# Kernel tuning notes

Hardware: AMD Instinct MI355X
Metric: run time of the kernel (lower is better)

## Reference

```python
import jax, jax.numpy as jnp
import numpy as np

EMB = 128
N_RBF = 16
N_EDGES = 1_000_000
N_ATOMS = 50_000


def setup_inputs() -> dict:
    key = jax.random.key(0)
    ks = jax.random.split(key, 16)
    inp = {
        "x": jax.random.normal(ks[0], (N_EDGES, EMB), dtype=jnp.float32),
        "rbf": jax.random.normal(ks[1], (N_EDGES, N_RBF), dtype=jnp.float32),
        "idnb_i": jax.random.randint(ks[2], (N_EDGES,), 0, N_ATOMS, dtype=jnp.int32),
        "n_atoms": N_ATOMS,
        # learned params
        "W_x": jax.random.normal(ks[3], (EMB, EMB), dtype=jnp.float32) * 0.05,
        "b_x": jnp.zeros((EMB,), dtype=jnp.float32),
        "W_rbf": jax.random.normal(ks[4], (N_RBF, EMB), dtype=jnp.float32) * 0.2,
        "b_rbf": jnp.zeros((EMB,), dtype=jnp.float32),
        "W1": jax.random.normal(ks[5], (EMB, EMB), dtype=jnp.float32) * 0.05,
        "b1": jnp.zeros((EMB,), dtype=jnp.float32),
        "W2": jax.random.normal(ks[6], (EMB, EMB), dtype=jnp.float32) * 0.05,
        "b2": jnp.zeros((EMB,), dtype=jnp.float32),
        "W3": jax.random.normal(ks[7], (EMB, EMB), dtype=jnp.float32) * 0.05,
        "b3": jnp.zeros((EMB,), dtype=jnp.float32),
        "W_final": jax.random.normal(ks[8], (EMB, 1), dtype=jnp.float32) * 0.05,
        # scale coefficients (shape [1] as in the keras layer)
        "coef_rbf_a": jnp.exp(jax.random.normal(ks[9], (1,)) * 0.01),
        "coef_rbf_b": jnp.exp(jax.random.normal(ks[10], (1,)) * 0.01),
        "coef_x": jnp.exp(jax.random.normal(ks[11], (1,)) * 0.01),
        "coef_final": jnp.exp(jax.random.normal(ks[12], (1,)) * 0.01),
    }
    return inp


def reference(x, rbf, idnb_i, n_atoms, W_x, b_x, W_rbf, b_rbf, W1, b1, W2, b2,
              W3, b3, W_final, coef_rbf_a, coef_rbf_b, coef_x, coef_final):
    act = jax.nn.silu  # keras 'swish'
    rbf = coef_rbf_a * rbf
    h = act(x @ W_x + b_x)                      # [E, emb]
    g = act(rbf @ W_rbf + b_rbf)                # [E, emb]
    conv_x = (coef_rbf_b * g) * (coef_x * h)    # fused elementwise gate
    a = jax.ops.segment_sum(conv_x, idnb_i, num_segments=n_atoms)  # [n_atoms, emb]
    a = act(a @ W1 + b1)
    a = act(a @ W2 + b2)
    a = act(a @ W3 + b3)
    out = (a @ W_final) * coef_final            # [n_atoms, 1]
    return out
```

## Files before the change

kernel.cpp:

```cpp
#include <hip/hip_runtime.h>

#define E_TOTAL 1000000
#define EMB     128
#define NRBF    16
#define NATOMS  50000
#define APB     16
#define NBLK    ((NATOMS + 255) / 256)

typedef _Float16 f16x8 __attribute__((ext_vector_type(8)));
typedef _Float16 f16x4 __attribute__((ext_vector_type(4)));
typedef float    f32x4 __attribute__((ext_vector_type(4)));

__device__ __forceinline__ float silu_f(float v) {
    return v * (1.0f / (1.0f + __expf(-v)));
}

__device__ __forceinline__ int sigma64(int e) {
    return (((e & 15) >> 2) << 4) + ((e >> 4) << 2) + (e & 3);
}

__global__ __launch_bounds__(256)
void hist_kernel(const int* __restrict__ idnb, int* __restrict__ counts) {
    const int e = blockIdx.x * 256 + threadIdx.x;
    if (e < E_TOTAL) atomicAdd(&counts[idnb[e]], 1);
}

__global__ __launch_bounds__(256)
void scan1_kernel(const int* __restrict__ counts, int* __restrict__ row_ptr,
                  int* __restrict__ bsums) {
    __shared__ int sd[256];
    const int tid = threadIdx.x;
    const int idx = blockIdx.x * 256 + tid;
    const int v = (idx < NATOMS) ? counts[idx] : 0;
    sd[tid] = v;
    __syncthreads();
#pragma unroll
    for (int off = 1; off < 256; off <<= 1) {
        const int t = (tid >= off) ? sd[tid - off] : 0;
        __syncthreads();
        sd[tid] += t;
        __syncthreads();
    }
    if (idx < NATOMS) row_ptr[idx] = sd[tid] - v;
    if (tid == 255) bsums[blockIdx.x] = sd[255];
}

__global__ __launch_bounds__(256)
void scan2_kernel(int* __restrict__ bsums) {
    __shared__ int sd[256];
    const int tid = threadIdx.x;
    const int v = (tid < NBLK) ? bsums[tid] : 0;
    sd[tid] = v;
    __syncthreads();
#pragma unroll
    for (int off = 1; off < 256; off <<= 1) {
        const int t = (tid >= off) ? sd[tid - off] : 0;
        __syncthreads();
        sd[tid] += t;
        __syncthreads();
    }
    if (tid < NBLK) bsums[tid] = sd[tid] - v;
}

__global__ __launch_bounds__(256)
void scan3_kernel(const int* __restrict__ bsums, int* __restrict__ row_ptr,
                  int* __restrict__ cursor) {
    const int idx = blockIdx.x * 256 + threadIdx.x;
    if (idx < NATOMS) {
        const int r = row_ptr[idx] + bsums[blockIdx.x];
        row_ptr[idx] = r;
        cursor[idx]  = r;
    }
    if (idx == 0) row_ptr[NATOMS] = E_TOTAL;
}

__global__ __launch_bounds__(256)
void scatter_kernel(const int* __restrict__ idnb, int* __restrict__ cursor,
                    int* __restrict__ eidx, int* __restrict__ aidxs) {
    const int e = blockIdx.x * 256 + threadIdx.x;
    if (e < E_TOTAL) {
        const int a = idnb[e];
        const int p = atomicAdd(&cursor[a], 1);
        eidx[p]  = e;
        aidxs[p] = a;
    }
}

__global__ __launch_bounds__(256, 2)
void edge_kernel(const float* __restrict__ x,
                 const float* __restrict__ rbf,
                 const int*   __restrict__ eidx,
                 const int*   __restrict__ aidxs,
                 const int*   __restrict__ row_ptr,
                 const float* __restrict__ Wx,
                 const float* __restrict__ bx,
                 const float* __restrict__ Wr,
                 const float* __restrict__ br,
                 const float* __restrict__ c_a,
                 const float* __restrict__ c_b,
                 const float* __restrict__ c_x,
                 float* __restrict__ acc)
{
    __shared__ _Float16 sX[2][64 * 128];
    __shared__ _Float16 sR[2][64 * 40];
    __shared__ float    sAcc[APB][132];
    __shared__ int      sAid[2][64];

    const int tid  = threadIdx.x;
    const int w    = tid >> 6;
    const int lane = tid & 63;
    const int lq   = lane >> 4;
    const int lm   = lane & 15;

    const int aBase = blockIdx.x * APB;
    const int eBeg  = row_ptr[aBase];
    const int eEnd  = row_ptr[aBase + APB];
    const int nEdge = eEnd - eBeg;
    const int ntile = (nEdge + 63) >> 6;

    const float ca = c_a[0];
    const float sc = c_b[0] * c_x[0];
    const int col0 = w * 32 + lm;
    const int col1 = col0 + 16;
    const float bx0 = bx[col0], bx1 = bx[col1];
    const float br0 = br[col0], br1 = br[col1];

    f16x8 wxh[4][2], wxl[4][2], wrh[2], wrl[2];
#pragma unroll
    for (int ks = 0; ks < 4; ++ks)
#pragma unroll
        for (int nt = 0; nt < 2; ++nt) {
            const int n = w * 32 + nt * 16 + lm;
            f16x8 h8, l8;
#pragma unroll
            for (int j = 0; j < 8; ++j) {
                const int k = ks * 32 + lq * 8 + j;
                const float v = Wx[k * EMB + n];
                const _Float16 hv = (_Float16)v;
                h8[j] = hv;
                l8[j] = (_Float16)(v - (float)hv);
            }
            wxh[ks][nt] = h8;
            wxl[ks][nt] = l8;
        }
#pragma unroll
    for (int nt = 0; nt < 2; ++nt) {
        const int n = w * 32 + nt * 16 + lm;
        f16x8 h8, l8;
#pragma unroll
        for (int j = 0; j < 8; ++j) {
            const int k = lq * 8 + j;
            const float v = (k < NRBF) ? Wr[k * EMB + n] : 0.f;
            const _Float16 hv = (_Float16)v;
            h8[j] = hv;
            l8[j] = (_Float16)(v - (float)hv);
        }
        wrh[nt] = h8;
        wrl[nt] = l8;
    }

    for (int f = tid; f < APB * 132; f += 256) ((float*)sAcc)[f] = 0.f;
    for (int f = tid; f < 64 * 24; f += 256) {
        sR[0][(f / 24) * 40 + 16 + (f % 24)] = (_Float16)0.f;
        sR[1][(f / 24) * 40 + 16 + (f % 24)] = (_Float16)0.f;
    }

    float4 px[8];
    float4 pr;
    int    prel = -1;

    auto prefetch = [&](int t) {
        const int nb = eBeg + t * 64;
#pragma unroll
        for (int i = 0; i < 8; ++i) {
            const int e = (tid >> 5) + i * 8;
            const int eid = eidx[min(nb + sigma64(e), eEnd - 1)];
            px[i] = *(const float4*)(x + (size_t)eid * EMB + (tid & 31) * 4);
        }
        {
            const int er = tid >> 2;
            const int eid = eidx[min(nb + sigma64(er), eEnd - 1)];
            pr = *(const float4*)(rbf + (size_t)eid * NRBF + (tid & 3) * 4);
        }
        if (tid < 64) prel = (nb + tid < eEnd) ? (aidxs[nb + tid] - aBase) : -1;
    };

    auto write_lds = [&](int buf) {
#pragma unroll
        for (int i = 0; i < 8; ++i) {
            const int e = (tid >> 5) + i * 8;
            const int kb = (tid & 31) * 4;
            const int idx = (e * 128 + kb) ^ ((e & 7) << 3);
            f16x4 h4 = {(_Float16)px[i].x, (_Float16)px[i].y,
                        (_Float16)px[i].z, (_Float16)px[i].w};
            *(f16x4*)&sX[buf][idx] = h4;
        }
        {
            const int er = tid >> 2;
            const int kb = (tid & 3) * 4;
            f16x4 r4 = {(_Float16)(pr.x * ca), (_Float16)(pr.y * ca),
                        (_Float16)(pr.z * ca), (_Float16)(pr.w * ca)};
            *(f16x4*)&sR[buf][er * 40 + kb] = r4;
        }
        if (tid < 64) sAid[buf][tid] = prel;
    };

    if (ntile > 0) {
        prefetch(0);
        write_lds(0);
        if (ntile > 1) prefetch(1);
    }
    __syncthreads();

    for (int t = 0; t < ntile; ++t) {
        const int cur = t & 1;
        const _Float16* sXc = sX[cur];
        const _Float16* sRc = sR[cur];
        const int*      sAc = sAid[cur];

        int   curA = -2;
        float a0v = 0.f, a1v = 0.f;

#pragma unroll
        for (int mt = 0; mt < 4; ++mt) {
            f32x4 hac[2], gac[2];
#pragma unroll
            for (int nt = 0; nt < 2; ++nt) { hac[nt] = 0.f; gac[nt] = 0.f; }

            const int m = mt * 16 + lm;
            const f16x8 rh = *(const f16x8*)&sRc[m * 40 + lq * 8];
#pragma unroll
            for (int nt = 0; nt < 2; ++nt) {
                gac[nt] = __builtin_amdgcn_mfma_f32_16x16x32_f16(rh, wrh[nt], gac[nt], 0, 0, 0);
                gac[nt] = __builtin_amdgcn_mfma_f32_16x16x32_f16(rh, wrl[nt], gac[nt], 0, 0, 0);
            }
#pragma unroll
            for (int ks = 0; ks < 4; ++ks) {
                const int xi = (m * 128 + ks * 32 + lq * 8) ^ ((m & 7) << 3);
                const f16x8 xh = *(const f16x8*)&sXc[xi];
#pragma unroll
                for (int nt = 0; nt < 2; ++nt) {
                    hac[nt] = __builtin_amdgcn_mfma_f32_16x16x32_f16(xh, wxh[ks][nt], hac[nt], 0, 0, 0);
                    hac[nt] = __builtin_amdgcn_mfma_f32_16x16x32_f16(xh, wxl[ks][nt], hac[nt], 0, 0, 0);
                }
            }

            const int pbase = lq * 16 + mt * 4;
            float v0[4], v1[4];
#pragma unroll
            for (int r = 0; r < 4; ++r) {
                const float g0 = gac[0][r] + br0, h0 = hac[0][r] + bx0;
                const float g1 = gac[1][r] + br1, h1 = hac[1][r] + bx1;
                const float d0 = (1.f + __expf(-g0)) * (1.f + __expf(-h0));
                const float d1 = (1.f + __expf(-g1)) * (1.f + __expf(-h1));
                v0[r] = sc * g0 * h0 * __builtin_amdgcn_rcpf(d0);
                v1[r] = sc * g1 * h1 * __builtin_amdgcn_rcpf(d1);
            }
#pragma unroll
            for (int r = 0; r < 4; ++r) {
                const int rel = sAc[pbase + r];
                if (rel != curA) {
                    if (curA >= 0) {
                        atomicAdd(&sAcc[curA][col0], a0v);
                        atomicAdd(&sAcc[curA][col1], a1v);
                    }
                    curA = rel; a0v = 0.f; a1v = 0.f;
                }
                a0v += v0[r];
                a1v += v1[r];
            }
        }
        if (curA >= 0) {
            atomicAdd(&sAcc[curA][col0], a0v);
            atomicAdd(&sAcc[curA][col1], a1v);
        }

        if (t + 1 < ntile) {
            write_lds((t + 1) & 1);
            if (t + 2 < ntile) prefetch(t + 2);
        }
        __syncthreads();
    }

    {
        const int r = tid >> 4;
        const int c = (tid & 15) * 8;
        float* dst = acc + (size_t)(aBase + r) * EMB + c;
        *(float4*)(dst)     = *(const float4*)&sAcc[r][c];
        *(float4*)(dst + 4) = *(const float4*)&sAcc[r][c + 4];
    }
}

__global__ __launch_bounds__(256, 2)
void layer_kernel(const float* __restrict__ X,
                  const float* __restrict__ W,
                  const float* __restrict__ b,
                  float* __restrict__ Y, int M)
{
    __shared__ _Float16 sX[64 * 128];

    const int tid  = threadIdx.x;
    const int w    = tid >> 6;
    const int lane = tid & 63;
    const int lq   = lane >> 4;
    const int lm   = lane & 15;

    const int col0 = w * 32 + lm;
    const int col1 = col0 + 16;
    const float b0 = b[col0], b1 = b[col1];

    f16x8 wh[4][2], wl[4][2];
#pragma unroll
    for (int ks = 0; ks < 4; ++ks)
#pragma unroll
        for (int nt = 0; nt < 2; ++nt) {
            const int n = w * 32 + nt * 16 + lm;
            f16x8 h8, l8;
#pragma unroll
            for (int j = 0; j < 8; ++j) {
                const int k = ks * 32 + lq * 8 + j;
                const float v = W[k * EMB + n];
                const _Float16 hv = (_Float16)v;
                h8[j] = hv;
                l8[j] = (_Float16)(v - (float)hv);
            }
            wh[ks][nt] = h8;
            wl[ks][nt] = l8;
        }

#pragma unroll
    for (int sub = 0; sub < 2; ++sub) {
        const int base = blockIdx.x * 128 + sub * 64;
        __syncthreads();
#pragma unroll
        for (int i = 0; i < 8; ++i) {
            const int e = (tid >> 5) + i * 8;
            const int row = min(base + e, M - 1);
            const float4 v = *(const float4*)(X + (size_t)row * EMB + (tid & 31) * 4);
            const int kb = (tid & 31) * 4;
            const int idx = (e * 128 + kb) ^ ((e & 7) << 3);
            f16x4 h4 = {(_Float16)v.x, (_Float16)v.y, (_Float16)v.z, (_Float16)v.w};
            *(f16x4*)&sX[idx] = h4;
        }
        __syncthreads();

#pragma unroll
        for (int mth = 0; mth < 2; ++mth) {
            f32x4 hac[2][2];
#pragma unroll
            for (int mi = 0; mi < 2; ++mi)
#pragma unroll
                for (int nt = 0; nt < 2; ++nt) hac[mi][nt] = 0.f;

#pragma unroll
            for (int mi = 0; mi < 2; ++mi) {
                const int m = (mth * 2 + mi) * 16 + lm;
#pragma unroll
                for (int ks = 0; ks < 4; ++ks) {
                    const int xi = (m * 128 + ks * 32 + lq * 8) ^ ((m & 7) << 3);
                    const f16x8 xh = *(const f16x8*)&sX[xi];
#pragma unroll
                    for (int nt = 0; nt < 2; ++nt) {
                        hac[mi][nt] = __builtin_amdgcn_mfma_f32_16x16x32_f16(xh, wh[ks][nt], hac[mi][nt], 0, 0, 0);
                        hac[mi][nt] = __builtin_amdgcn_mfma_f32_16x16x32_f16(xh, wl[ks][nt], hac[mi][nt], 0, 0, 0);
                    }
                }
            }
#pragma unroll
            for (int mi = 0; mi < 2; ++mi) {
                const int rb = base + (mth * 2 + mi) * 16 + lq * 4;
#pragma unroll
                for (int r = 0; r < 4; ++r) {
                    const int row = rb + r;
                    if (row < M) {
                        Y[(size_t)row * EMB + col0] = silu_f(hac[mi][0][r] + b0);
                        Y[(size_t)row * EMB + col1] = silu_f(hac[mi][1][r] + b1);
                    }
                }
            }
        }
    }
}

__global__ __launch_bounds__(256, 2)
void layer3_final_kernel(const float* __restrict__ X,
                         const float* __restrict__ W,
                         const float* __restrict__ b,
                         const float* __restrict__ Wf,
                         const float* __restrict__ cf,
                         float* __restrict__ out, int M)
{
    __shared__ _Float16 sX[64 * 128];
    __shared__ float    sOut[128];

    const int tid  = threadIdx.x;
    const int w    = tid >> 6;
    const int lane = tid & 63;
    const int lq   = lane >> 4;
    const int lm   = lane & 15;

    const int col0 = w * 32 + lm;
    const int col1 = col0 + 16;
    const float b0 = b[col0], b1 = b[col1];
    const float wf0 = Wf[col0], wf1 = Wf[col1];
    const float cfv = cf[0];

    if (tid < 128) sOut[tid] = 0.f;

    f16x8 wh[4][2], wl[4][2];
#pragma unroll
    for (int ks = 0; ks < 4; ++ks)
#pragma unroll
        for (int nt = 0; nt < 2; ++nt) {
            const int n = w * 32 + nt * 16 + lm;
            f16x8 h8, l8;
#pragma unroll
            for (int j = 0; j < 8; ++j) {
                const int k = ks * 32 + lq * 8 + j;
                const float v = W[k * EMB + n];
                const _Float16 hv = (_Float16)v;
                h8[j] = hv;
                l8[j] = (_Float16)(v - (float)hv);
            }
            wh[ks][nt] = h8;
            wl[ks][nt] = l8;
        }

#pragma unroll
    for (int sub = 0; sub < 2; ++sub) {
        const int base = blockIdx.x * 128 + sub * 64;
        __syncthreads();
#pragma unroll
        for (int i = 0; i < 8; ++i) {
            const int e = (tid >> 5) + i * 8;
            const int row = min(base + e, M - 1);
            const float4 v = *(const float4*)(X + (size_t)row * EMB + (tid & 31) * 4);
            const int kb = (tid & 31) * 4;
            const int idx = (e * 128 + kb) ^ ((e & 7) << 3);
            f16x4 h4 = {(_Float16)v.x, (_Float16)v.y, (_Float16)v.z, (_Float16)v.w};
            *(f16x4*)&sX[idx] = h4;
        }
        __syncthreads();

#pragma unroll
        for (int mth = 0; mth < 2; ++mth) {
            f32x4 hac[2][2];
#pragma unroll
            for (int mi = 0; mi < 2; ++mi)
#pragma unroll
                for (int nt = 0; nt < 2; ++nt) hac[mi][nt] = 0.f;

#pragma unroll
            for (int mi = 0; mi < 2; ++mi) {
                const int m = (mth * 2 + mi) * 16 + lm;
#pragma unroll
                for (int ks = 0; ks < 4; ++ks) {
                    const int xi = (m * 128 + ks * 32 + lq * 8) ^ ((m & 7) << 3);
                    const f16x8 xh = *(const f16x8*)&sX[xi];
#pragma unroll
                    for (int nt = 0; nt < 2; ++nt) {
                        hac[mi][nt] = __builtin_amdgcn_mfma_f32_16x16x32_f16(xh, wh[ks][nt], hac[mi][nt], 0, 0, 0);
                        hac[mi][nt] = __builtin_amdgcn_mfma_f32_16x16x32_f16(xh, wl[ks][nt], hac[mi][nt], 0, 0, 0);
                    }
                }
            }
#pragma unroll
            for (int mi = 0; mi < 2; ++mi) {
                const int lrow = sub * 64 + (mth * 2 + mi) * 16 + lq * 4;
#pragma unroll
                for (int r = 0; r < 4; ++r) {
                    const float o0 = silu_f(hac[mi][0][r] + b0);
                    const float o1 = silu_f(hac[mi][1][r] + b1);
                    float p = o0 * wf0 + o1 * wf1;
#pragma unroll
                    for (int off = 1; off < 16; off <<= 1)
                        p += __shfl_xor(p, off);
                    if (lm == 0 && base + (mth * 2 + mi) * 16 + lq * 4 + r < M)
                        atomicAdd(&sOut[lrow + r], p);
                }
            }
        }
    }

    __syncthreads();
    if (tid < 128) {
        const int row = blockIdx.x * 128 + tid;
        if (row < M) out[row] = sOut[tid] * cfv;
    }
}

extern "C" void kernel_launch(void* const* d_in, const int* in_sizes, int n_in,
                              void* d_out, int out_size, void* d_ws, size_t ws_size,
                              hipStream_t stream) {
    const float* x    = (const float*)d_in[0];
    const float* rbf  = (const float*)d_in[1];
    const int*   idnb = (const int*)  d_in[2];
    const float* Wx   = (const float*)d_in[4];
    const float* bx   = (const float*)d_in[5];
    const float* Wr   = (const float*)d_in[6];
    const float* brf  = (const float*)d_in[7];
    const float* W1   = (const float*)d_in[8];
    const float* b1   = (const float*)d_in[9];
    const float* W2   = (const float*)d_in[10];
    const float* b2   = (const float*)d_in[11];
    const float* W3   = (const float*)d_in[12];
    const float* b3   = (const float*)d_in[13];
    const float* Wf   = (const float*)d_in[14];
    const float* c_a  = (const float*)d_in[15];
    const float* c_b  = (const float*)d_in[16];
    const float* c_x  = (const float*)d_in[17];
    const float* c_f  = (const float*)d_in[18];

    float* out = (float*)d_out;
    float* acc = (float*)d_ws;
    float* buf = acc + (size_t)NATOMS * EMB;
    int* eidx    = (int*)buf;
    int* aidxs   = eidx + E_TOTAL;
    int* counts  = aidxs + E_TOTAL;
    int* row_ptr = counts + NATOMS;
    int* cursor  = row_ptr + NATOMS + 1;
    int* bsums   = cursor + NATOMS;

    hipMemsetAsync(counts, 0, NATOMS * sizeof(int), stream);

    hist_kernel<<<(E_TOTAL + 255) / 256, 256, 0, stream>>>(idnb, counts);
    scan1_kernel<<<NBLK, 256, 0, stream>>>(counts, row_ptr, bsums);
    scan2_kernel<<<1, 256, 0, stream>>>(bsums);
    scan3_kernel<<<NBLK, 256, 0, stream>>>(bsums, row_ptr, cursor);
    scatter_kernel<<<(E_TOTAL + 255) / 256, 256, 0, stream>>>(idnb, cursor, eidx, aidxs);

    edge_kernel<<<NATOMS / APB, 256, 0, stream>>>(x, rbf, eidx, aidxs, row_ptr,
                                                  Wx, bx, Wr, brf,
                                                  c_a, c_b, c_x, acc);

    const int ltiles = (NATOMS + 127) / 128;
    layer_kernel<<<ltiles, 256, 0, stream>>>(acc, W1, b1, buf, NATOMS);
    layer_kernel<<<ltiles, 256, 0, stream>>>(buf, W2, b2, acc, NATOMS);
    layer3_final_kernel<<<ltiles, 256, 0, stream>>>(acc, W3, b3, Wf, c_f, out, NATOMS);
}
```

Baseline: 421.4 us.

## Derive edge atom ids from row_ptr and single-buffer LDS in edge kernel

Drops the aidxs array: the scatter kernel no longer writes per-edge atom ids, and the edge kernel recomputes each edge's local atom index by comparing its position against 16 cached row_ptr values. LDS staging goes from double to single buffering, with two barriers per tile around the LDS write, while the next tile's global loads are still issued ahead into registers. The MFMA work is regrouped so two m-tiles are computed before their epilogues, which may improve instruction overlap. This saves a 4 MB write and read plus LDS space, at the cost of an extra barrier per tile and extra registers for the row_ptr cache.

Measured after the change: 399.4 us. -5.2%, faster.

```diff
diff --git a/kernel.cpp b/kernel.cpp
--- a/kernel.cpp
+++ b/kernel.cpp
@@ -76,13 +76,12 @@
 
 __global__ __launch_bounds__(256)
 void scatter_kernel(const int* __restrict__ idnb, int* __restrict__ cursor,
-                    int* __restrict__ eidx, int* __restrict__ aidxs) {
+                    int* __restrict__ eidx) {
     const int e = blockIdx.x * 256 + threadIdx.x;
     if (e < E_TOTAL) {
         const int a = idnb[e];
         const int p = atomicAdd(&cursor[a], 1);
-        eidx[p]  = e;
-        aidxs[p] = a;
+        eidx[p] = e;
     }
 }
 
@@ -90,7 +89,6 @@
 void edge_kernel(const float* __restrict__ x,
                  const float* __restrict__ rbf,
                  const int*   __restrict__ eidx,
-                 const int*   __restrict__ aidxs,
                  const int*   __restrict__ row_ptr,
                  const float* __restrict__ Wx,
                  const float* __restrict__ bx,
@@ -101,10 +99,10 @@
                  const float* __restrict__ c_x,
                  float* __restrict__ acc)
 {
-    __shared__ _Float16 sX[2][64 * 128];
-    __shared__ _Float16 sR[2][64 * 40];
+    __shared__ _Float16 sX[64 * 128];
+    __shared__ _Float16 sR[64 * 40];
     __shared__ float    sAcc[APB][132];
-    __shared__ int      sAid[2][64];
+    __shared__ int      sAid[64];
 
     const int tid  = threadIdx.x;
     const int w    = tid >> 6;
@@ -113,8 +111,12 @@
     const int lm   = lane & 15;
 
     const int aBase = blockIdx.x * APB;
-    const int eBeg  = row_ptr[aBase];
-    const int eEnd  = row_ptr[aBase + APB];
+
+    int rp[APB];
+#pragma unroll
+    for (int a = 0; a < APB; ++a) rp[a] = row_ptr[aBase + a];
+    const int eBeg = rp[0];
+    const int eEnd = row_ptr[aBase + APB];
     const int nEdge = eEnd - eBeg;
     const int ntile = (nEdge + 63) >> 6;
 
@@ -160,10 +162,8 @@
     }
 
     for (int f = tid; f < APB * 132; f += 256) ((float*)sAcc)[f] = 0.f;
-    for (int f = tid; f < 64 * 24; f += 256) {
-        sR[0][(f / 24) * 40 + 16 + (f % 24)] = (_Float16)0.f;
-        sR[1][(f / 24) * 40 + 16 + (f % 24)] = (_Float16)0.f;
-    }
+    for (int f = tid; f < 64 * 24; f += 256)
+        sR[(f / 24) * 40 + 16 + (f % 24)] = (_Float16)0.f;
 
     float4 px[8];
     float4 pr;
@@ -182,10 +182,20 @@
             const int eid = eidx[min(nb + sigma64(er), eEnd - 1)];
             pr = *(const float4*)(rbf + (size_t)eid * NRBF + (tid & 3) * 4);
         }
-        if (tid < 64) prel = (nb + tid < eEnd) ? (aidxs[nb + tid] - aBase) : -1;
+        if (tid < 64) {
+            const int pos = nb + tid;
+            if (pos >= eEnd) {
+                prel = -1;
+            } else {
+                int rel = 0;
+#pragma unroll
+                for (int a = 1; a < APB; ++a) rel += (pos >= rp[a]) ? 1 : 0;
+                prel = rel;
+            }
+        }
     };
 
-    auto write_lds = [&](int buf) {
+    auto write_lds = [&]() {
 #pragma unroll
         for (int i = 0; i < 8; ++i) {
             const int e = (tid >> 5) + i * 8;
@@ -193,58 +203,30 @@
             const int idx = (e * 128 + kb) ^ ((e & 7) << 3);
             f16x4 h4 = {(_Float16)px[i].x, (_Float16)px[i].y,
                         (_Float16)px[i].z, (_Float16)px[i].w};
-            *(f16x4*)&sX[buf][idx] = h4;
+            *(f16x4*)&sX[idx] = h4;
         }
         {
             const int er = tid >> 2;
             const int kb = (tid & 3) * 4;
             f16x4 r4 = {(_Float16)(pr.x * ca), (_Float16)(pr.y * ca),
                         (_Float16)(pr.z * ca), (_Float16)(pr.w * ca)};
-            *(f16x4*)&sR[buf][er * 40 + kb] = r4;
-        }
-        if (tid < 64) sAid[buf][tid] = prel;
+            *(f16x4*)&sR[er * 40 + kb] = r4;
+        }
+        if (tid < 64) sAid[tid] = prel;
     };
 
-    if (ntile > 0) {
-        prefetch(0);
-        write_lds(0);
-        if (ntile > 1) prefetch(1);
-    }
-    __syncthreads();
+    if (ntile > 0) prefetch(0);
 
     for (int t = 0; t < ntile; ++t) {
-        const int cur = t & 1;
-        const _Float16* sXc = sX[cur];
-        const _Float16* sRc = sR[cur];
-        const int*      sAc = sAid[cur];
+        __syncthreads();
+        write_lds();
+        __syncthreads();
+        if (t + 1 < ntile) prefetch(t + 1);
 
         int   curA = -2;
         float a0v = 0.f, a1v = 0.f;
 
-#pragma unroll
-        for (int mt = 0; mt < 4; ++mt) {
-            f32x4 hac[2], gac[2];
-#pragma unroll
-            for (int nt = 0; nt < 2; ++nt) { hac[nt] = 0.f; gac[nt] = 0.f; }
-
-            const int m = mt * 16 + lm;
-            const f16x8 rh = *(const f16x8*)&sRc[m * 40 + lq * 8];
-#pragma unroll
-            for (int nt = 0; nt < 2; ++nt) {
-                gac[nt] = __builtin_amdgcn_mfma_f32_16x16x32_f16(rh, wrh[nt], gac[nt], 0, 0, 0);
-                gac[nt] = __builtin_amdgcn_mfma_f32_16x16x32_f16(rh, wrl[nt], gac[nt], 0, 0, 0);
-            }
-#pragma unroll
-            for (int ks = 0; ks < 4; ++ks) {
-                const int xi = (m * 128 + ks * 32 + lq * 8) ^ ((m & 7) << 3);
-                const f16x8 xh = *(const f16x8*)&sXc[xi];
-#pragma unroll
-                for (int nt = 0; nt < 2; ++nt) {
-                    hac[nt] = __builtin_amdgcn_mfma_f32_16x16x32_f16(xh, wxh[ks][nt], hac[nt], 0, 0, 0);
-                    hac[nt] = __builtin_amdgcn_mfma_f32_16x16x32_f16(xh, wxl[ks][nt], hac[nt], 0, 0, 0);
-                }
-            }
-
+        auto epi = [&](const f32x4 hac[2], const f32x4 gac[2], int mt) {
             const int pbase = lq * 16 + mt * 4;
             float v0[4], v1[4];
 #pragma unroll
@@ -258,7 +240,7 @@
             }
 #pragma unroll
             for (int r = 0; r < 4; ++r) {
-                const int rel = sAc[pbase + r];
+                const int rel = sAid[pbase + r];
                 if (rel != curA) {
                     if (curA >= 0) {
                         atomicAdd(&sAcc[curA][col0], a0v);
@@ -269,19 +251,46 @@
                 a0v += v0[r];
                 a1v += v1[r];
             }
-        }
+        };
+
+        auto mfma_mt = [&](f32x4 hac[2], f32x4 gac[2], int mt) {
+#pragma unroll
+            for (int nt = 0; nt < 2; ++nt) { hac[nt] = 0.f; gac[nt] = 0.f; }
+            const int m = mt * 16 + lm;
+            const f16x8 rh = *(const f16x8*)&sR[m * 40 + lq * 8];
+#pragma unroll
+            for (int nt = 0; nt < 2; ++nt) {
+                gac[nt] = __builtin_amdgcn_mfma_f32_16x16x32_f16(rh, wrh[nt], gac[nt], 0, 0, 0);
+                gac[nt] = __builtin_amdgcn_mfma_f32_16x16x32_f16(rh, wrl[nt], gac[nt], 0, 0, 0);
+            }
+#pragma unroll
+            for (int ks = 0; ks < 4; ++ks) {
+                const int xi = (m * 128 + ks * 32 + lq * 8) ^ ((m & 7) << 3);
+                const f16x8 xh = *(const f16x8*)&sX[xi];
+#pragma unroll
+                for (int nt = 0; nt < 2; ++nt) {
+                    hac[nt] = __builtin_amdgcn_mfma_f32_16x16x32_f16(xh, wxh[ks][nt], hac[nt], 0, 0, 0);
+                    hac[nt] = __builtin_amdgcn_mfma_f32_16x16x32_f16(xh, wxl[ks][nt], hac[nt], 0, 0, 0);
+                }
+            }
+        };
+
+#pragma unroll
+        for (int g = 0; g < 2; ++g) {
+            f32x4 hacA[2], gacA[2], hacB[2], gacB[2];
+            mfma_mt(hacA, gacA, g * 2);
+            mfma_mt(hacB, gacB, g * 2 + 1);
+            epi(hacA, gacA, g * 2);
+            epi(hacB, gacB, g * 2 + 1);
+        }
+
         if (curA >= 0) {
             atomicAdd(&sAcc[curA][col0], a0v);
             atomicAdd(&sAcc[curA][col1], a1v);
         }
-
-        if (t + 1 < ntile) {
-            write_lds((t + 1) & 1);
-            if (t + 2 < ntile) prefetch(t + 2);
-        }
-        __syncthreads();
-    }
-
+    }
+
+    __syncthreads();
     {
         const int r = tid >> 4;
         const int c = (tid & 15) * 8;
@@ -515,8 +524,7 @@
     float* acc = (float*)d_ws;
     float* buf = acc + (size_t)NATOMS * EMB;
     int* eidx    = (int*)buf;
-    int* aidxs   = eidx + E_TOTAL;
-    int* counts  = aidxs + E_TOTAL;
+    int* counts  = eidx + E_TOTAL;
     int* row_ptr = counts + NATOMS;
     int* cursor  = row_ptr + NATOMS + 1;
     int* bsums   = cursor + NATOMS;
@@ -527,9 +535,9 @@
     scan1_kernel<<<NBLK, 256, 0, stream>>>(counts, row_ptr, bsums);
     scan2_kernel<<<1, 256, 0, stream>>>(bsums);
     scan3_kernel<<<NBLK, 256, 0, stream>>>(bsums, row_ptr, cursor);
-    scatter_kernel<<<(E_TOTAL + 255) / 256, 256, 0, stream>>>(idnb, cursor, eidx, aidxs);
-
-    edge_kernel<<<NATOMS / APB, 256, 0, stream>>>(x, rbf, eidx, aidxs, row_ptr,
+    scatter_kernel<<<(E_TOTAL + 255) / 256, 256, 0, stream>>>(idnb, cursor, eidx);
+
+    edge_kernel<<<NATOMS / APB, 256, 0, stream>>>(x, rbf, eidx, row_ptr,
                                                   Wx, bx, Wr, brf,
                                                   c_a, c_b, c_x, acc);
 
```
